# Optimization experiments

Hardware: AMD Instinct MI355X
Metric: run time of the kernel (lower is better)

## Reference

```python
import jax, jax.numpy as jnp
import numpy as np
from jax import lax

NUM_ITER = 40


def _pool(x, win, op, init):
    pads = [(0, 0), (0, 0)] + [(w // 2, w // 2) for w in win]
    return lax.reduce_window(x, init, op, (1, 1) + win, (1, 1, 1, 1, 1), pads)


def soft_erode(x):
    # -maxpool(-x) with zero-effect padding == min-pool padded with +inf.
    inf = jnp.asarray(jnp.inf, x.dtype)
    p1 = _pool(x, (3, 1, 1), lax.min, inf)
    p2 = _pool(x, (1, 3, 1), lax.min, inf)
    p3 = _pool(x, (1, 1, 3), lax.min, inf)
    return jnp.minimum(jnp.minimum(p1, p2), p3)


def soft_dilate(x):
    return _pool(x, (3, 3, 3), lax.max, jnp.asarray(-jnp.inf, x.dtype))


def soft_open(x):
    return soft_dilate(soft_erode(x))


def setup_inputs() -> dict:
    key = jax.random.key(0)
    img = jax.random.uniform(key, (2, 1, 192, 192, 192), dtype=jnp.float32)
    return {"img": img}


def reference(img):
    skeleton = jax.nn.relu(img - soft_open(img))

    def body(_, carry):
        im, skel = carry
        im = soft_erode(im)
        delta = jax.nn.relu(im - soft_open(im))
        skel = skel + jax.nn.relu(delta - skel * delta)
        return (im, skel)

    _, skeleton = lax.fori_loop(0, NUM_ITER, body, (img, skeleton))
    return skeleton
```

## Files before the change

kernel.cpp:

```cpp
#include <hip/hip_runtime.h>


#define Dn 192
#define Hn 192
#define Wn 192
#define PLANE (Hn * Wn)
#define TOTAL_ELEMS (2 * Dn * Hn * Wn)
#define NYG (Hn / 4)
#define ZPT 8
#define ZC (Dn / ZPT)
#define NBLK (NYG * ZC * 2)
#define NITER2 (ZPT + 6)
#define NITER1 (ZPT + 4)

static __device__ __forceinline__ void lds_barrier() {
    asm volatile("s_waitcnt lgkmcnt(0)" ::: "memory");
    __builtin_amdgcn_s_barrier();
}

typedef _Float16 h2 __attribute__((ext_vector_type(2)));
typedef _Float16 h4 __attribute__((ext_vector_type(4)));

static __device__ __forceinline__ h2 h2min(h2 a, h2 b) { return __builtin_elementwise_min(a, b); }
static __device__ __forceinline__ h2 h2max(h2 a, h2 b) { return __builtin_elementwise_max(a, b); }
static __device__ __forceinline__ h2 h2min3(h2 a, h2 b, h2 c) { return h2min(h2min(a, b), c); }
static __device__ __forceinline__ h2 h2max3(h2 a, h2 b, h2 c) { return h2max(h2max(a, b), c); }
static __device__ __forceinline__ unsigned int u32(h2 v) { return __builtin_bit_cast(unsigned int, v); }
static __device__ __forceinline__ h2 h2c(unsigned int v) { return __builtin_bit_cast(h2, v); }

template <int CHUNK>
__device__ __forceinline__ int swizzle(int bid) {
    return (bid & 7) * CHUNK + (bid >> 3);
}

template <bool FIRST>
__global__ __launch_bounds__(192, 4) void fused2_k(const void* __restrict__ X_,
                                                   const _Float16* Sin,
                                                   _Float16* Sout,
                                                   _Float16* __restrict__ Aout) {
    const float* Xf = (const float*)X_;
    const _Float16* Xh = (const _Float16*)X_;

    const int bid = swizzle<NBLK / 8>((int)blockIdx.x);
    const int gy = bid % NYG;
    const int t2 = bid / NYG;
    const int zc = t2 % ZC;
    const int b = t2 / ZC;
    const int x = threadIdx.x;
    const int y0 = gy * 4;
    const int z0 = zc * ZPT;
    const int cbase = b * (Dn * PLANE) + y0 * Wn + x;

    int roff[10];
#pragma unroll
    for (int k = 0; k < 10; ++k) {
        int ry = y0 - 3 + k;
        ry = ry < 0 ? 0 : (ry > Hn - 1 ? Hn - 1 : ry);
        roff[k] = (ry - y0) * Wn;
    }

    __shared__ unsigned int sh[2][192][11];
    const int xu = (x < Wn - 1) ? x + 1 : x;
    const int xd = (x > 0) ? x - 1 : x;

    h2 aM1[4] = {}, aM2[4] = {}, hmM1[4] = {}, aUM1[4] = {}, aDM1[4] = {};
    h2 e1M1t[3] = {}, e1M2t[3] = {}, hm1M1[3] = {}, e1UM1[3] = {}, e1DM1[3] = {};
    h2 m1M1[2] = {}, m1M2[2] = {}, m1M3[2] = {};
    h2 m2M1[2] = {}, m2M2[2] = {};
    h2 xcM1[2] = {}, xcM2[2] = {}, xcM3[2] = {};
    h2 e1cM1[2] = {}, e1cM2[2] = {}, e2cM1[2] = {};
    h4 sP = {};

    _Float16 hP[10];
    float fP[10];
    auto issue = [&](int p) {
        int pz = p < 0 ? 0 : (p > Dn - 1 ? Dn - 1 : p);
        if (FIRST) {
            const float* pp = Xf + cbase + pz * PLANE;
#pragma unroll
            for (int k = 0; k < 10; ++k) fP[k] = pp[roff[k]];
        } else {
            const _Float16* pp = Xh + cbase + pz * PLANE;
#pragma unroll
            for (int k = 0; k < 10; ++k) hP[k] = pp[roff[k]];
        }
    };
    issue(z0 - 3);

#pragma unroll
    for (int i = 0; i < NITER2; ++i) {
        const int p = z0 - 3 + i;
        const int zo = p - 3;

        _Float16 s[10];
#pragma unroll
        for (int k = 0; k < 10; ++k) s[k] = FIRST ? (_Float16)fP[k] : hP[k];

        if (i + 1 < NITER2) issue(p + 1);

        h4 sN = {};
        if (!FIRST && i >= 5 && i + 1 < NITER2) {
            const _Float16* sp = Sin + cbase + (p - 2) * PLANE;
            sN.x = sp[0]; sN.y = sp[Wn]; sN.z = sp[2 * Wn]; sN.w = sp[3 * Wn];
        }

        h2 P[9];
#pragma unroll
        for (int k = 0; k < 9; ++k) { h2 t = {s[k], s[k + 1]}; P[k] = t; }
        h2 a0[4] = {P[1], P[3], P[5], P[7]};
        h2 hm0[4];
#pragma unroll
        for (int j = 0; j < 4; ++j)
            hm0[j] = h2min3(P[2 * j], P[2 * j + 1], P[2 * j + 2]);
        h2 xc0[2] = {P[3], P[5]};

        h2 e1[4] = {}, t[3] = {}, hm1_0[3] = {}, e1c0[2] = {};
        if (i >= 2) {
#pragma unroll
            for (int k = 0; k < 4; ++k)
                e1[k] = h2min3(h2min(hmM1[k], aM2[k]),
                               h2min(aUM1[k], aDM1[k]), a0[k]);
            if (gy == 0) { h2 v = {e1[1].x, e1[1].x}; e1[0] = v; }
            if (gy == NYG - 1) { h2 v = {e1[2].y, e1[2].y}; e1[3] = v; }
            t[0] = __builtin_shufflevector(e1[0], e1[1], 1, 2);
            t[1] = __builtin_shufflevector(e1[1], e1[2], 1, 2);
            t[2] = __builtin_shufflevector(e1[2], e1[3], 1, 2);
            hm1_0[0] = h2min3(e1[0], t[0], e1[1]);
            hm1_0[1] = h2min3(e1[1], t[1], e1[2]);
            hm1_0[2] = h2min3(e1[2], t[2], e1[3]);
            e1c0[0] = e1[1]; e1c0[1] = e1[2];
        }

        h2 e2[3] = {}, e2c0[2] = {};
        if (i >= 4) {
#pragma unroll
            for (int j = 0; j < 3; ++j)
                e2[j] = h2min3(h2min(hm1M1[j], e1M2t[j]),
                               h2min(e1UM1[j], e1DM1[j]), t[j]);
            if (gy == 0) { h2 v = {e2[0].y, e2[0].y}; e2[0] = v; }
            if (gy == NYG - 1) { h2 v = {e2[2].x, e2[2].x}; e2[2] = v; }
            e2c0[0] = __builtin_shufflevector(e2[0], e2[1], 1, 2);
            e2c0[1] = __builtin_shufflevector(e2[1], e2[2], 1, 2);
        }

        const int sl = i & 1;
#pragma unroll
        for (int k = 0; k < 4; ++k) sh[sl][x][k] = u32(a0[k]);
        if (i >= 2) {
#pragma unroll
            for (int j = 0; j < 3; ++j) sh[sl][x][4 + j] = u32(t[j]);
        }
        if (i >= 4) {
#pragma unroll
            for (int j = 0; j < 3; ++j) sh[sl][x][7 + j] = u32(e2[j]);
        }
        lds_barrier();
        h2 aU0[4], aD0[4];
#pragma unroll
        for (int k = 0; k < 4; ++k) {
            aU0[k] = h2c(sh[sl][xu][k]);
            aD0[k] = h2c(sh[sl][xd][k]);
        }
        h2 tU[3] = {}, tD[3] = {}, m1_0[2] = {}, m2_0[2] = {};
        if (i >= 2) {
#pragma unroll
            for (int j = 0; j < 3; ++j) {
                tU[j] = h2c(sh[sl][xu][4 + j]);
                tD[j] = h2c(sh[sl][xd][4 + j]);
            }
            h2 vm0 = h2max3(t[0], tU[0], tD[0]);
            h2 vm1 = h2max3(t[1], tU[1], tD[1]);
            h2 vm2 = h2max3(t[2], tU[2], tD[2]);
            h2 mid01 = __builtin_shufflevector(vm0, vm1, 1, 2);
            h2 mid23 = __builtin_shufflevector(vm1, vm2, 1, 2);
            m1_0[0] = h2max3(vm0, mid01, vm1);
            m1_0[1] = h2max3(vm1, mid23, vm2);
        }
        if (i >= 4) {
            h2 eU0 = h2c(sh[sl][xu][7]), eU1 = h2c(sh[sl][xu][8]), eU2 = h2c(sh[sl][xu][9]);
            h2 eD0 = h2c(sh[sl][xd][7]), eD1 = h2c(sh[sl][xd][8]), eD2 = h2c(sh[sl][xd][9]);
            h2 vm0 = h2max3(e2[0], eU0, eD0);
            h2 vm1 = h2max3(e2[1], eU1, eD1);
            h2 vm2 = h2max3(e2[2], eU2, eD2);
            h2 mid01 = __builtin_shufflevector(vm0, vm1, 1, 2);
            h2 mid23 = __builtin_shufflevector(vm1, vm2, 1, 2);
            m2_0[0] = h2max3(vm0, mid01, vm1);
            m2_0[1] = h2max3(vm1, mid23, vm2);
        }

        if (i >= 6) {
            const int offo = cbase + zo * PLANE;
            const bool zlo = (zo == 0);
            const bool zhi = (zo == Dn - 1);
            h2 d1a0 = zlo ? m1M2[0] : m1M3[0];
            h2 d1a1 = zlo ? m1M2[1] : m1M3[1];
            h2 d1c0 = zhi ? m1M2[0] : m1M1[0];
            h2 d1c1 = zhi ? m1M2[1] : m1M1[1];
            h2 D1_0 = h2max3(d1a0, m1M2[0], d1c0);
            h2 D1_1 = h2max3(d1a1, m1M2[1], d1c1);
            h2 d2a0 = zlo ? m2M1[0] : m2M2[0];
            h2 d2a1 = zlo ? m2M1[1] : m2M2[1];
            h2 d2c0 = zhi ? m2M1[0] : m2_0[0];
            h2 d2c1 = zhi ? m2M1[1] : m2_0[1];
            h2 D2_0 = h2max3(d2a0, m2M1[0], d2c0);
            h2 D2_1 = h2max3(d2a1, m2M1[1], d2c1);

            float ex[4] = {(float)xcM3[0].x, (float)xcM3[0].y,
                           (float)xcM3[1].x, (float)xcM3[1].y};
            float e1v[4] = {(float)e1cM2[0].x, (float)e1cM2[0].y,
                            (float)e1cM2[1].x, (float)e1cM2[1].y};
            float d1[4] = {(float)D1_0.x, (float)D1_0.y, (float)D1_1.x, (float)D1_1.y};
            float d2[4] = {(float)D2_0.x, (float)D2_0.y, (float)D2_1.x, (float)D2_1.y};
            float sv[4] = {(float)sP.x, (float)sP.y, (float)sP.z, (float)sP.w};
#pragma unroll
            for (int q = 0; q < 4; ++q) {
                float de1 = fmaxf(ex[q] - d1[q], 0.f);
                float s1 = FIRST ? de1 : (sv[q] + fmaxf(de1 - sv[q] * de1, 0.f));
                float de2 = fmaxf(e1v[q] - d2[q], 0.f);
                sv[q] = s1 + fmaxf(de2 - s1 * de2, 0.f);
            }
            Sout[offo] = (_Float16)sv[0];
            Sout[offo + Wn] = (_Float16)sv[1];
            Sout[offo + 2 * Wn] = (_Float16)sv[2];
            Sout[offo + 3 * Wn] = (_Float16)sv[3];
            Aout[offo] = e2cM1[0].x;
            Aout[offo + Wn] = e2cM1[0].y;
            Aout[offo + 2 * Wn] = e2cM1[1].x;
            Aout[offo + 3 * Wn] = e2cM1[1].y;
        }

#pragma unroll
        for (int k = 0; k < 4; ++k) {
            aM2[k] = aM1[k]; aM1[k] = a0[k];
            hmM1[k] = hm0[k]; aUM1[k] = aU0[k]; aDM1[k] = aD0[k];
        }
#pragma unroll
        for (int j = 0; j < 3; ++j) {
            e1M2t[j] = e1M1t[j]; e1M1t[j] = t[j];
            hm1M1[j] = hm1_0[j]; e1UM1[j] = tU[j]; e1DM1[j] = tD[j];
        }
        m1M3[0] = m1M2[0]; m1M3[1] = m1M2[1];
        m1M2[0] = m1M1[0]; m1M2[1] = m1M1[1];
        m1M1[0] = m1_0[0]; m1M1[1] = m1_0[1];
        m2M2[0] = m2M1[0]; m2M2[1] = m2M1[1];
        m2M1[0] = m2_0[0]; m2M1[1] = m2_0[1];
        xcM3[0] = xcM2[0]; xcM3[1] = xcM2[1];
        xcM2[0] = xcM1[0]; xcM2[1] = xcM1[1];
        xcM1[0] = xc0[0];  xcM1[1] = xc0[1];
        e1cM2[0] = e1cM1[0]; e1cM2[1] = e1cM1[1];
        e1cM1[0] = e1c0[0]; e1cM1[1] = e1c0[1];
        e2cM1[0] = e2c0[0]; e2cM1[1] = e2c0[1];
        sP = sN;
    }
}

template <bool FIRST, bool LAST>
__global__ __launch_bounds__(192, 4) void step_k(const void* __restrict__ X_,
                                                 const _Float16* Sin,
                                                 void* Sout_,
                                                 _Float16* __restrict__ Aout) {
    const float* Xf = (const float*)X_;
    const _Float16* Xh = (const _Float16*)X_;
    _Float16* Sh = (_Float16*)Sout_;
    float* Sf = (float*)Sout_;

    const int bid = swizzle<NBLK / 8>((int)blockIdx.x);
    const int gy = bid % NYG;
    const int t2 = bid / NYG;
    const int zc = t2 % ZC;
    const int b = t2 / ZC;
    const int x = threadIdx.x;
    const int y0 = gy * 4;
    const int z0 = zc * ZPT;
    const int cbase = b * (Dn * PLANE) + y0 * Wn + x;

    int roff[8];
#pragma unroll
    for (int k = 0; k < 8; ++k) {
        int ry = y0 - 2 + k;
        ry = ry < 0 ? 0 : (ry > Hn - 1 ? Hn - 1 : ry);
        roff[k] = (ry - y0) * Wn;
    }

    __shared__ unsigned int sh[2][192][7];
    const int xu = (x < Wn - 1) ? x + 1 : x;
    const int xd = (x > 0) ? x - 1 : x;

    h2 aM2[3], aM1[3], hmM1[3], aUM1[3], aDM1[3];
    h2 xcM1[2], xcM2[2], e1cM1[2], mM1[2], mM2[2];

    _Float16 hP[8];
    float fP[8];
    h4 sP = {};

    auto issue = [&](int p) {
        int pz = p < 0 ? 0 : (p > Dn - 1 ? Dn - 1 : p);
        if (FIRST) {
            const float* pp = Xf + cbase + pz * PLANE;
#pragma unroll
            for (int k = 0; k < 8; ++k) fP[k] = pp[roff[k]];
        } else {
            const _Float16* pp = Xh + cbase + pz * PLANE;
#pragma unroll
            for (int k = 0; k < 8; ++k) hP[k] = pp[roff[k]];
        }
    };
    issue(z0 - 2);

#pragma unroll
    for (int i = 0; i < NITER1; ++i) {
        const int p = z0 - 2 + i;
        const int zo = p - 2;

        _Float16 s[8];
#pragma unroll
        for (int k = 0; k < 8; ++k) s[k] = FIRST ? (_Float16)fP[k] : hP[k];

        if (i + 1 < NITER1) issue(p + 1);

        h4 sN = {};
        if (!FIRST && i >= 3 && i + 1 < NITER1) {
            const _Float16* sp = Sin + cbase + (p - 1) * PLANE;
            sN.x = sp[0]; sN.y = sp[Wn]; sN.z = sp[2 * Wn]; sN.w = sp[3 * Wn];
        }

        h2 P[7];
#pragma unroll
        for (int k = 0; k < 7; ++k) { h2 t = {s[k], s[k + 1]}; P[k] = t; }
        h2 a0[3] = {P[1], P[3], P[5]};
        h2 hm0[3];
#pragma unroll
        for (int j = 0; j < 3; ++j)
            hm0[j] = h2min3(P[2 * j], P[2 * j + 1], P[2 * j + 2]);
        h2 xc0[2] = {P[2], P[4]};

        h2 e1[3];
        if (i >= 2) {
#pragma unroll
            for (int k = 0; k < 3; ++k)
                e1[k] = h2min3(h2min(hmM1[k], aM2[k]),
                               h2min(aUM1[k], aDM1[k]), a0[k]);
            if (gy == 0)       e1[0] = __builtin_shufflevector(e1[0], e1[0], 1, 1);
            if (gy == NYG - 1) e1[2] = __builtin_shufflevector(e1[2], e1[2], 0, 0);
        }

        const int sl = i & 1;
        sh[sl][x][0] = u32(a0[0]);
        sh[sl][x][1] = u32(a0[1]);
        sh[sl][x][2] = u32(a0[2]);
        if (i >= 2) {
            sh[sl][x][3] = u32(e1[0]);
            sh[sl][x][4] = u32(e1[1]);
            sh[sl][x][5] = u32(e1[2]);
        }
        lds_barrier();
        h2 aU0[3] = {h2c(sh[sl][xu][0]), h2c(sh[sl][xu][1]), h2c(sh[sl][xu][2])};
        h2 aD0[3] = {h2c(sh[sl][xd][0]), h2c(sh[sl][xd][1]), h2c(sh[sl][xd][2])};

        h2 m0[2], e1c0[2];
        if (i >= 2) {
            h2 eU0 = h2c(sh[sl][xu][3]), eU1 = h2c(sh[sl][xu][4]), eU2 = h2c(sh[sl][xu][5]);
            h2 eD0 = h2c(sh[sl][xd][3]), eD1 = h2c(sh[sl][xd][4]), eD2 = h2c(sh[sl][xd][5]);
            h2 vm0 = h2max3(e1[0], eU0, eD0);
            h2 vm1 = h2max3(e1[1], eU1, eD1);
            h2 vm2 = h2max3(e1[2], eU2, eD2);
            h2 mid01 = __builtin_shufflevector(vm0, vm1, 1, 2);
            h2 mid23 = __builtin_shufflevector(vm1, vm2, 1, 2);
            m0[0] = h2max3(vm0, mid01, vm1);
            m0[1] = h2max3(vm1, mid23, vm2);
            e1c0[0] = __builtin_shufflevector(e1[0], e1[1], 1, 2);
            e1c0[1] = __builtin_shufflevector(e1[1], e1[2], 1, 2);
        }

        if (i >= 4) {
            const int offo = cbase + zo * PLANE;
            const bool zlo = (zo == 0);
            const bool zhi = (zo == Dn - 1);
            h2 mzA0 = zlo ? mM1[0] : mM2[0];
            h2 mzA1 = zlo ? mM1[1] : mM2[1];
            h2 mzC0 = zhi ? mM1[0] : m0[0];
            h2 mzC1 = zhi ? mM1[1] : m0[1];
            h2 d01 = h2max3(mzA0, mM1[0], mzC0);
            h2 d23 = h2max3(mzA1, mM1[1], mzC1);

            float ex0 = (float)xcM2[0].x, ex1 = (float)xcM2[0].y;
            float ex2 = (float)xcM2[1].x, ex3 = (float)xcM2[1].y;
            float de0 = fmaxf(ex0 - (float)d01.x, 0.f);
            float de1 = fmaxf(ex1 - (float)d01.y, 0.f);
            float de2 = fmaxf(ex2 - (float)d23.x, 0.f);
            float de3 = fmaxf(ex3 - (float)d23.y, 0.f);
            float s0, s1, s2, s3;
            if (FIRST) {
                s0 = de0; s1 = de1; s2 = de2; s3 = de3;
            } else {
                s0 = (float)sP.x; s1 = (float)sP.y;
                s2 = (float)sP.z; s3 = (float)sP.w;
                s0 += fmaxf(de0 - s0 * de0, 0.f);
                s1 += fmaxf(de1 - s1 * de1, 0.f);
                s2 += fmaxf(de2 - s2 * de2, 0.f);
                s3 += fmaxf(de3 - s3 * de3, 0.f);
            }
            if (LAST) {
                Sf[offo] = s0; Sf[offo + Wn] = s1;
                Sf[offo + 2 * Wn] = s2; Sf[offo + 3 * Wn] = s3;
            } else {
                Sh[offo] = (_Float16)s0;
                Sh[offo + Wn] = (_Float16)s1;
                Sh[offo + 2 * Wn] = (_Float16)s2;
                Sh[offo + 3 * Wn] = (_Float16)s3;
                Aout[offo] = e1cM1[0].x;
                Aout[offo + Wn] = e1cM1[0].y;
                Aout[offo + 2 * Wn] = e1cM1[1].x;
                Aout[offo + 3 * Wn] = e1cM1[1].y;
            }
        }

#pragma unroll
        for (int k = 0; k < 3; ++k) {
            aM2[k] = aM1[k]; aM1[k] = a0[k];
            hmM1[k] = hm0[k]; aUM1[k] = aU0[k]; aDM1[k] = aD0[k];
        }
        xcM2[0] = xcM1[0]; xcM2[1] = xcM1[1];
        xcM1[0] = xc0[0];  xcM1[1] = xc0[1];
        if (i >= 2) {
            mM2[0] = mM1[0]; mM2[1] = mM1[1];
            mM1[0] = m0[0];  mM1[1] = m0[1];
            e1cM1[0] = e1c0[0]; e1cM1[1] = e1c0[1];
        }
        sP = sN;
    }
}

extern "C" void kernel_launch(void* const* d_in, const int* in_sizes, int n_in,
                              void* d_out, int out_size, void* d_ws, size_t ws_size,
                              hipStream_t stream) {
    const float* img = (const float*)d_in[0];
    _Float16* B0 = (_Float16*)d_ws;
    _Float16* B1 = B0 + TOTAL_ELEMS;
    _Float16* S  = B1 + TOTAL_ELEMS;

    fused2_k<true><<<NBLK, 192, 0, stream>>>(img, nullptr, S, B0);
    _Float16* a = B0;
    _Float16* nb = B1;
    for (int j = 0; j < 19; ++j) {
        fused2_k<false><<<NBLK, 192, 0, stream>>>(a, S, S, nb);
        _Float16* t = a; a = nb; nb = t;
    }
    step_k<false, true><<<NBLK, 192, 0, stream>>>(a, S, d_out, nullptr);
}
```

Measured before the change: 930.1 us.

## Deepen z-prefetch to two planes, single-buffer LDS, enlarge z-chunk per block

Each block now covers 12 depth planes instead of 8, which cuts the redundant halo planes recomputed per block. Global loads are issued two planes ahead from a double-buffered register array, to hide more memory latency. The double-buffered shared array becomes a single buffer guarded by a second barrier per iteration, which frees LDS, and launch bounds ask for 5 waves per SIMD. The cost is more register pressure and an extra barrier per plane, and the larger chunk gives fewer blocks (ZC drops from 24 to 16).

```diff
diff --git a/kernel.cpp b/kernel.cpp
--- a/kernel.cpp
+++ b/kernel.cpp
@@ -7,7 +7,7 @@
 #define PLANE (Hn * Wn)
 #define TOTAL_ELEMS (2 * Dn * Hn * Wn)
 #define NYG (Hn / 4)
-#define ZPT 8
+#define ZPT 12
 #define ZC (Dn / ZPT)
 #define NBLK (NYG * ZC * 2)
 #define NITER2 (ZPT + 6)
@@ -34,7 +34,7 @@
 }
 
 template <bool FIRST>
-__global__ __launch_bounds__(192, 4) void fused2_k(const void* __restrict__ X_,
+__global__ __launch_bounds__(192, 5) void fused2_k(const void* __restrict__ X_,
                                                    const _Float16* Sin,
                                                    _Float16* Sout,
                                                    _Float16* __restrict__ Aout) {
@@ -59,7 +59,7 @@
         roff[k] = (ry - y0) * Wn;
     }
 
-    __shared__ unsigned int sh[2][192][11];
+    __shared__ unsigned int sh[192][11];
     const int xu = (x < Wn - 1) ? x + 1 : x;
     const int xd = (x > 0) ? x - 1 : x;
 
@@ -71,32 +71,34 @@
     h2 e1cM1[2] = {}, e1cM2[2] = {}, e2cM1[2] = {};
     h4 sP = {};
 
-    _Float16 hP[10];
-    float fP[10];
-    auto issue = [&](int p) {
+    _Float16 hP[2][10];
+    float fP[2][10];
+    auto issue = [&](int p, int buf) {
         int pz = p < 0 ? 0 : (p > Dn - 1 ? Dn - 1 : p);
         if (FIRST) {
             const float* pp = Xf + cbase + pz * PLANE;
 #pragma unroll
-            for (int k = 0; k < 10; ++k) fP[k] = pp[roff[k]];
+            for (int k = 0; k < 10; ++k) fP[buf][k] = pp[roff[k]];
         } else {
             const _Float16* pp = Xh + cbase + pz * PLANE;
 #pragma unroll
-            for (int k = 0; k < 10; ++k) hP[k] = pp[roff[k]];
+            for (int k = 0; k < 10; ++k) hP[buf][k] = pp[roff[k]];
         }
     };
-    issue(z0 - 3);
+    issue(z0 - 3, 0);
+    issue(z0 - 2, 1);
 
 #pragma unroll
     for (int i = 0; i < NITER2; ++i) {
         const int p = z0 - 3 + i;
         const int zo = p - 3;
+        const int pb = i & 1;
 
         _Float16 s[10];
 #pragma unroll
-        for (int k = 0; k < 10; ++k) s[k] = FIRST ? (_Float16)fP[k] : hP[k];
-
-        if (i + 1 < NITER2) issue(p + 1);
+        for (int k = 0; k < 10; ++k) s[k] = FIRST ? (_Float16)fP[pb][k] : hP[pb][k];
+
+        if (i + 2 < NITER2) issue(p + 2, pb);
 
         h4 sN = {};
         if (!FIRST && i >= 5 && i + 1 < NITER2) {
@@ -143,31 +145,42 @@
             e2c0[1] = __builtin_shufflevector(e2[1], e2[2], 1, 2);
         }
 
-        const int sl = i & 1;
-#pragma unroll
-        for (int k = 0; k < 4; ++k) sh[sl][x][k] = u32(a0[k]);
-        if (i >= 2) {
-#pragma unroll
-            for (int j = 0; j < 3; ++j) sh[sl][x][4 + j] = u32(t[j]);
+#pragma unroll
+        for (int k = 0; k < 4; ++k) sh[x][k] = u32(a0[k]);
+        if (i >= 2) {
+#pragma unroll
+            for (int j = 0; j < 3; ++j) sh[x][4 + j] = u32(t[j]);
         }
         if (i >= 4) {
 #pragma unroll
-            for (int j = 0; j < 3; ++j) sh[sl][x][7 + j] = u32(e2[j]);
+            for (int j = 0; j < 3; ++j) sh[x][7 + j] = u32(e2[j]);
         }
         lds_barrier();
         h2 aU0[4], aD0[4];
 #pragma unroll
         for (int k = 0; k < 4; ++k) {
-            aU0[k] = h2c(sh[sl][xu][k]);
-            aD0[k] = h2c(sh[sl][xd][k]);
-        }
-        h2 tU[3] = {}, tD[3] = {}, m1_0[2] = {}, m2_0[2] = {};
+            aU0[k] = h2c(sh[xu][k]);
+            aD0[k] = h2c(sh[xd][k]);
+        }
+        h2 tU[3] = {}, tD[3] = {}, eUr[3] = {}, eDr[3] = {};
         if (i >= 2) {
 #pragma unroll
             for (int j = 0; j < 3; ++j) {
-                tU[j] = h2c(sh[sl][xu][4 + j]);
-                tD[j] = h2c(sh[sl][xd][4 + j]);
+                tU[j] = h2c(sh[xu][4 + j]);
+                tD[j] = h2c(sh[xd][4 + j]);
             }
+        }
+        if (i >= 4) {
+#pragma unroll
+            for (int j = 0; j < 3; ++j) {
+                eUr[j] = h2c(sh[xu][7 + j]);
+                eDr[j] = h2c(sh[xd][7 + j]);
+            }
+        }
+        lds_barrier();
+
+        h2 m1_0[2] = {}, m2_0[2] = {};
+        if (i >= 2) {
             h2 vm0 = h2max3(t[0], tU[0], tD[0]);
             h2 vm1 = h2max3(t[1], tU[1], tD[1]);
             h2 vm2 = h2max3(t[2], tU[2], tD[2]);
@@ -177,11 +190,9 @@
             m1_0[1] = h2max3(vm1, mid23, vm2);
         }
         if (i >= 4) {
-            h2 eU0 = h2c(sh[sl][xu][7]), eU1 = h2c(sh[sl][xu][8]), eU2 = h2c(sh[sl][xu][9]);
-            h2 eD0 = h2c(sh[sl][xd][7]), eD1 = h2c(sh[sl][xd][8]), eD2 = h2c(sh[sl][xd][9]);
-            h2 vm0 = h2max3(e2[0], eU0, eD0);
-            h2 vm1 = h2max3(e2[1], eU1, eD1);
-            h2 vm2 = h2max3(e2[2], eU2, eD2);
+            h2 vm0 = h2max3(e2[0], eUr[0], eDr[0]);
+            h2 vm1 = h2max3(e2[1], eUr[1], eDr[1]);
+            h2 vm2 = h2max3(e2[2], eUr[2], eDr[2]);
             h2 mid01 = __builtin_shufflevector(vm0, vm1, 1, 2);
             h2 mid23 = __builtin_shufflevector(vm1, vm2, 1, 2);
             m2_0[0] = h2max3(vm0, mid01, vm1);
@@ -255,7 +266,7 @@
 }
 
 template <bool FIRST, bool LAST>
-__global__ __launch_bounds__(192, 4) void step_k(const void* __restrict__ X_,
+__global__ __launch_bounds__(192, 5) void step_k(const void* __restrict__ X_,
                                                  const _Float16* Sin,
                                                  void* Sout_,
                                                  _Float16* __restrict__ Aout) {
@@ -282,41 +293,43 @@
         roff[k] = (ry - y0) * Wn;
     }
 
-    __shared__ unsigned int sh[2][192][7];
+    __shared__ unsigned int sh[192][7];
     const int xu = (x < Wn - 1) ? x + 1 : x;
     const int xd = (x > 0) ? x - 1 : x;
 
-    h2 aM2[3], aM1[3], hmM1[3], aUM1[3], aDM1[3];
-    h2 xcM1[2], xcM2[2], e1cM1[2], mM1[2], mM2[2];
-
-    _Float16 hP[8];
-    float fP[8];
+    h2 aM2[3] = {}, aM1[3] = {}, hmM1[3] = {}, aUM1[3] = {}, aDM1[3] = {};
+    h2 xcM1[2] = {}, xcM2[2] = {}, e1cM1[2] = {}, mM1[2] = {}, mM2[2] = {};
+
+    _Float16 hP[2][8];
+    float fP[2][8];
     h4 sP = {};
 
-    auto issue = [&](int p) {
+    auto issue = [&](int p, int buf) {
         int pz = p < 0 ? 0 : (p > Dn - 1 ? Dn - 1 : p);
         if (FIRST) {
             const float* pp = Xf + cbase + pz * PLANE;
 #pragma unroll
-            for (int k = 0; k < 8; ++k) fP[k] = pp[roff[k]];
+            for (int k = 0; k < 8; ++k) fP[buf][k] = pp[roff[k]];
         } else {
             const _Float16* pp = Xh + cbase + pz * PLANE;
 #pragma unroll
-            for (int k = 0; k < 8; ++k) hP[k] = pp[roff[k]];
+            for (int k = 0; k < 8; ++k) hP[buf][k] = pp[roff[k]];
         }
     };
-    issue(z0 - 2);
+    issue(z0 - 2, 0);
+    issue(z0 - 1, 1);
 
 #pragma unroll
     for (int i = 0; i < NITER1; ++i) {
         const int p = z0 - 2 + i;
         const int zo = p - 2;
+        const int pb = i & 1;
 
         _Float16 s[8];
 #pragma unroll
-        for (int k = 0; k < 8; ++k) s[k] = FIRST ? (_Float16)fP[k] : hP[k];
-
-        if (i + 1 < NITER1) issue(p + 1);
+        for (int k = 0; k < 8; ++k) s[k] = FIRST ? (_Float16)fP[pb][k] : hP[pb][k];
+
+        if (i + 2 < NITER1) issue(p + 2, pb);
 
         h4 sN = {};
         if (!FIRST && i >= 3 && i + 1 < NITER1) {
@@ -334,7 +347,7 @@
             hm0[j] = h2min3(P[2 * j], P[2 * j + 1], P[2 * j + 2]);
         h2 xc0[2] = {P[2], P[4]};
 
-        h2 e1[3];
+        h2 e1[3] = {};
         if (i >= 2) {
 #pragma unroll
             for (int k = 0; k < 3; ++k)
@@ -344,23 +357,26 @@
             if (gy == NYG - 1) e1[2] = __builtin_shufflevector(e1[2], e1[2], 0, 0);
         }
 
-        const int sl = i & 1;
-        sh[sl][x][0] = u32(a0[0]);
-        sh[sl][x][1] = u32(a0[1]);
-        sh[sl][x][2] = u32(a0[2]);
-        if (i >= 2) {
-            sh[sl][x][3] = u32(e1[0]);
-            sh[sl][x][4] = u32(e1[1]);
-            sh[sl][x][5] = u32(e1[2]);
+        sh[x][0] = u32(a0[0]);
+        sh[x][1] = u32(a0[1]);
+        sh[x][2] = u32(a0[2]);
+        if (i >= 2) {
+            sh[x][3] = u32(e1[0]);
+            sh[x][4] = u32(e1[1]);
+            sh[x][5] = u32(e1[2]);
         }
         lds_barrier();
-        h2 aU0[3] = {h2c(sh[sl][xu][0]), h2c(sh[sl][xu][1]), h2c(sh[sl][xu][2])};
-        h2 aD0[3] = {h2c(sh[sl][xd][0]), h2c(sh[sl][xd][1]), h2c(sh[sl][xd][2])};
-
-        h2 m0[2], e1c0[2];
-        if (i >= 2) {
-            h2 eU0 = h2c(sh[sl][xu][3]), eU1 = h2c(sh[sl][xu][4]), eU2 = h2c(sh[sl][xu][5]);
-            h2 eD0 = h2c(sh[sl][xd][3]), eD1 = h2c(sh[sl][xd][4]), eD2 = h2c(sh[sl][xd][5]);
+        h2 aU0[3] = {h2c(sh[xu][0]), h2c(sh[xu][1]), h2c(sh[xu][2])};
+        h2 aD0[3] = {h2c(sh[xd][0]), h2c(sh[xd][1]), h2c(sh[xd][2])};
+        h2 eU0 = {}, eU1 = {}, eU2 = {}, eD0 = {}, eD1 = {}, eD2 = {};
+        if (i >= 2) {
+            eU0 = h2c(sh[xu][3]); eU1 = h2c(sh[xu][4]); eU2 = h2c(sh[xu][5]);
+            eD0 = h2c(sh[xd][3]); eD1 = h2c(sh[xd][4]); eD2 = h2c(sh[xd][5]);
+        }
+        lds_barrier();
+
+        h2 m0[2] = {}, e1c0[2] = {};
+        if (i >= 2) {
             h2 vm0 = h2max3(e1[0], eU0, eD0);
             h2 vm1 = h2max3(e1[1], eU1, eD1);
             h2 vm2 = h2max3(e1[2], eU2, eD2);
```

New measurement: 1.869 ms. +101.0%, slower.
